# Performance work log

Hardware: AMD Instinct MI355X
Metric: run time of the kernel (lower is better)

Reference implementation:

```python
import jax, jax.numpy as jnp
import numpy as np

EMBED_DIM = 64  # scale factor dim (matches head dim)


def setup_inputs() -> dict:
    key0 = jax.random.key(0)
    kq, kk, kv = jax.random.split(key0, 3)
    shape = (2, 16, 2048, 64)  # [B, H, S, D]
    return {
        "query": jax.random.normal(kq, shape, dtype=jnp.float32),
        "key": jax.random.normal(kk, shape, dtype=jnp.float32),
        "value": jax.random.normal(kv, shape, dtype=jnp.float32),
    }


def reference(query, key, value):
    # qk = Q K^T / sqrt(embed_dim); softmax over last dim; @ V
    inv_scale = jnp.sqrt(jnp.asarray(EMBED_DIM, dtype=query.dtype))
    scores = jnp.einsum("bhqd,bhkd->bhqk", query, key) / inv_scale
    probs = jax.nn.softmax(scores, axis=-1)
    # dropout_p=0.0 -> identity (eval semantics)
    return jnp.einsum("bhqk,bhkd->bhqd", probs, value)
```

## Files before the change

### kernel.cpp

```cpp
#include <hip/hip_runtime.h>
#include <hip/hip_bf16.h>

#define S_LEN 2048
#define DDIM  64
#define NT    (S_LEN / 64)
#define SCALE  0.125f
#define SCALE2 0.18033688f
#define NELEM  4194304
#define NQROW  65536

typedef __attribute__((ext_vector_type(8))) short short8;
typedef __attribute__((ext_vector_type(4))) short short4v;
typedef __attribute__((ext_vector_type(4))) float floatx4;

__device__ __forceinline__ short f2bf(float f) {
    union { float f; unsigned u; } v; v.f = f;
    return (short)((v.u + 0x7fffu + ((v.u >> 16) & 1u)) >> 16);
}

__device__ __forceinline__ float fexp2(float x) {
#if __has_builtin(__builtin_amdgcn_exp2f)
    return __builtin_amdgcn_exp2f(x);
#else
    return exp2f(x);
#endif
}

__device__ __forceinline__ void dma16(const void* g, void* l) {
    __builtin_amdgcn_global_load_lds(
        (const __attribute__((address_space(1))) void*)g,
        (__attribute__((address_space(3))) void*)l, 16, 0, 0);
}

__global__ __launch_bounds__(256) void prep_kv(const float* __restrict__ K,
                                               const float* __restrict__ V,
                                               short* __restrict__ Kb,
                                               short* __restrict__ Vt) {
    __shared__ short T[64 * 68];
    const int bh = blockIdx.x & 31;
    const int st = blockIdx.x >> 5;
    const int t  = threadIdx.x;
    const size_t tile_off = (size_t)bh * (S_LEN * DDIM) + (size_t)st * (64 * DDIM);

    {
        const float* src = K + tile_off + t * 16;
        short* dst = Kb + tile_off + t * 16;
        #pragma unroll
        for (int h = 0; h < 2; ++h) {
            float4 a = *(const float4*)(src + h * 8);
            float4 b = *(const float4*)(src + h * 8 + 4);
            short8 o;
            o[0]=f2bf(a.x); o[1]=f2bf(a.y); o[2]=f2bf(a.z); o[3]=f2bf(a.w);
            o[4]=f2bf(b.x); o[5]=f2bf(b.y); o[6]=f2bf(b.z); o[7]=f2bf(b.w);
            *(short8*)(dst + h * 8) = o;
        }
    }

    const float* src = V + tile_off;
    const int skey = t >> 2, scol = (t & 3) * 4;
    #pragma unroll
    for (int i = 0; i < 4; ++i) {
        const int c = scol + i * 16;
        float4 v = *(const float4*)(src + (size_t)skey * 64 + c);
        short4v o; o[0]=f2bf(v.x); o[1]=f2bf(v.y); o[2]=f2bf(v.z); o[3]=f2bf(v.w);
        *(short4v*)&T[skey * 68 + c] = o;
    }
    __syncthreads();
    const int d = t >> 2, cb = (t & 3) * 16;
    short8 o0, o1;
    #pragma unroll
    for (int j = 0; j < 8; ++j) {
        o0[j] = T[(cb + j) * 68 + d];
        o1[j] = T[(cb + 8 + j) * 68 + d];
    }
    short* dst = Vt + (size_t)bh * (DDIM * S_LEN) + (size_t)d * S_LEN + st * 64 + cb;
    *(short8*)dst       = o0;
    *(short8*)(dst + 8) = o1;
}

template <int NSPLIT>
__global__ __launch_bounds__(256) void attn_sm(
    const float* __restrict__ Q, const short* __restrict__ Kb,
    const short* __restrict__ Vt, float* __restrict__ O,
    float* __restrict__ numer, float* __restrict__ denom)
{
    __shared__ short Ks[2][64 * 64];
    __shared__ short Vs[2][64 * 64];
    __shared__ short Pl[4][32 * 64];

    constexpr int NIT = NT / NSPLIT;

    const int tid  = threadIdx.x;
    const int wave = tid >> 6;
    const int lane = tid & 63;
    const int l16  = lane & 15;
    const int quad = lane >> 4;
    const int x7   = l16 & 7;

    const int bh = blockIdx.x & 31;
    const int rest = blockIdx.x >> 5;
    const int qt = rest & 15;
    const int ks = rest >> 4;
    const size_t base = (size_t)bh * (S_LEN * DDIM);

    const int ci0 = tid,        r0 = ci0 >> 3, c0 = (ci0 & 7) ^ (r0 & 7);
    const int ci1 = 256 + tid,  r1 = ci1 >> 3, c1 = (ci1 & 7) ^ (r1 & 7);
    const size_t koff = (size_t)ks * NIT * (64 * 64);
    const size_t voff = (size_t)ks * NIT * 64;
    const short* pK0 = Kb + base + koff + r0 * 64 + c0 * 8;
    const short* pK1 = Kb + base + koff + r1 * 64 + c1 * 8;
    const short* pV0 = Vt + base + voff + (size_t)r0 * S_LEN + c0 * 8;
    const short* pV1 = Vt + base + voff + (size_t)r1 * S_LEN + c1 * 8;

    dma16(pK0, &Ks[0][ci0 * 8]);
    dma16(pK1, &Ks[0][ci1 * 8]);
    dma16(pV0, &Vs[0][ci0 * 8]);
    dma16(pV1, &Vs[0][ci1 * 8]);

    short8 qf[2][2];
    #pragma unroll
    for (int nq = 0; nq < 2; ++nq) {
        const float* qp = Q + base + (size_t)(qt * 128 + wave * 32 + nq * 16 + l16) * 64 + quad * 8;
        #pragma unroll
        for (int kt = 0; kt < 2; ++kt) {
            float4 a = *(const float4*)(qp + kt * 32);
            float4 b = *(const float4*)(qp + kt * 32 + 4);
            short* d = (short*)&qf[nq][kt];
            d[0]=f2bf(a.x*SCALE2); d[1]=f2bf(a.y*SCALE2); d[2]=f2bf(a.z*SCALE2); d[3]=f2bf(a.w*SCALE2);
            d[4]=f2bf(b.x*SCALE2); d[5]=f2bf(b.y*SCALE2); d[6]=f2bf(b.z*SCALE2); d[7]=f2bf(b.w*SCALE2);
        }
    }

    floatx4 oacc[2][4];
    float rs[2];
    #pragma unroll
    for (int mt = 0; mt < 2; ++mt) {
        #pragma unroll
        for (int dt = 0; dt < 4; ++dt) oacc[mt][dt] = (floatx4){0.f,0.f,0.f,0.f};
        rs[mt] = 0.f;
    }

    short* Pw = &Pl[wave][0];

    for (int kb = 0; kb < NIT; ++kb) {
        const int cur = kb & 1;
        __syncthreads();

        if (kb + 1 < NIT) {
            const int nxt = cur ^ 1;
            const int ok = (kb + 1) * (64 * 64), ov = (kb + 1) * 64;
            dma16(pK0 + ok, &Ks[nxt][ci0 * 8]);
            dma16(pK1 + ok, &Ks[nxt][ci1 * 8]);
            dma16(pV0 + ov, &Vs[nxt][ci0 * 8]);
            dma16(pV1 + ov, &Vs[nxt][ci1 * 8]);
        }

        const short* ks_ = Ks[cur];
        floatx4 sc[2][4];
        #pragma unroll
        for (int mk = 0; mk < 4; ++mk) {
            floatx4 a0 = (floatx4){0.f,0.f,0.f,0.f};
            floatx4 a1 = (floatx4){0.f,0.f,0.f,0.f};
            #pragma unroll
            for (int kt = 0; kt < 2; ++kt) {
                const int csw = (kt * 4 + quad) ^ x7;
                short8 kf = *(const short8*)&ks_[(mk * 16 + l16) * 64 + csw * 8];
                a0 = __builtin_amdgcn_mfma_f32_16x16x32_bf16(kf, qf[0][kt], a0, 0, 0, 0);
                a1 = __builtin_amdgcn_mfma_f32_16x16x32_bf16(kf, qf[1][kt], a1, 0, 0, 0);
            }
            sc[0][mk] = a0; sc[1][mk] = a1;
        }

        #pragma unroll
        for (int nq = 0; nq < 2; ++nq) {
            const int prow = (nq * 16 + l16) * 64;
            #pragma unroll
            for (int mk = 0; mk < 4; ++mk) {
                float p0 = fexp2(sc[nq][mk][0]);
                float p1 = fexp2(sc[nq][mk][1]);
                float p2 = fexp2(sc[nq][mk][2]);
                float p3 = fexp2(sc[nq][mk][3]);
                rs[nq] += (p0 + p1) + (p2 + p3);
                short4v pv;
                pv[0]=f2bf(p0); pv[1]=f2bf(p1); pv[2]=f2bf(p2); pv[3]=f2bf(p3);
                const int c8 = (mk * 4 + quad) ^ (2 * x7);
                *(short4v*)&Pw[prow + c8 * 4] = pv;
            }
        }

        const short* vs = Vs[cur];
        #pragma unroll
        for (int kt = 0; kt < 2; ++kt) {
            const int csw = (kt * 4 + quad) ^ x7;
            short8 pf0 = *(const short8*)&Pw[(l16)      * 64 + csw * 8];
            short8 pf1 = *(const short8*)&Pw[(16 + l16) * 64 + csw * 8];
            #pragma unroll
            for (int dt = 0; dt < 4; ++dt) {
                short8 vf = *(const short8*)&vs[(dt * 16 + l16) * 64 + csw * 8];
                oacc[0][dt] = __builtin_amdgcn_mfma_f32_16x16x32_bf16(pf0, vf, oacc[0][dt], 0, 0, 0);
                oacc[1][dt] = __builtin_amdgcn_mfma_f32_16x16x32_bf16(pf1, vf, oacc[1][dt], 0, 0, 0);
            }
        }
    }

    float inv[2];
    #pragma unroll
    for (int nq = 0; nq < 2; ++nq) {
        float s = rs[nq];
        s += __shfl_xor(s, 16, 64);
        s += __shfl_xor(s, 32, 64);
        if (NSPLIT == 2) {
            if (quad == 0)
                denom[(size_t)ks * NQROW + bh * S_LEN + qt * 128 + wave * 32 + nq * 16 + l16] = s;
        }
        inv[nq] = 1.0f / s;
    }

    #pragma unroll
    for (int mt = 0; mt < 2; ++mt) {
        const float dv = (NSPLIT == 1) ? __shfl(inv[mt], quad * 4, 64) : 0.f;
        #pragma unroll
        for (int r = 0; r < 4; ++r) {
            const int row = qt * 128 + wave * 32 + mt * 16 + quad * 4 + r;
            if (NSPLIT == 1) {
                const float d_r = __shfl(inv[mt], quad * 4 + r, 64);
                float* op = O + base + (size_t)row * 64 + l16;
                #pragma unroll
                for (int dt = 0; dt < 4; ++dt)
                    op[dt * 16] = oacc[mt][dt][r] * d_r;
            } else {
                float* np = numer + (size_t)ks * NELEM + base + (size_t)row * 64 + l16;
                #pragma unroll
                for (int dt = 0; dt < 4; ++dt)
                    np[dt * 16] = oacc[mt][dt][r];
            }
        }
        (void)dv;
    }
}

__global__ __launch_bounds__(256) void combine2(const float* __restrict__ numer,
                                                const float* __restrict__ denom,
                                                float* __restrict__ O) {
    const size_t i = ((size_t)blockIdx.x * 256 + threadIdx.x) * 4;
    const size_t q = i >> 6;
    const float inv = 1.0f / (denom[q] + denom[NQROW + q]);
    float4 n0 = *(const float4*)(numer + i);
    float4 n1 = *(const float4*)(numer + NELEM + i);
    float4 o;
    o.x = (n0.x + n1.x) * inv;
    o.y = (n0.y + n1.y) * inv;
    o.z = (n0.z + n1.z) * inv;
    o.w = (n0.w + n1.w) * inv;
    *(float4*)(O + i) = o;
}

#define BQ    64
#define BKEY  64
#define KPAD  72

__global__ __launch_bounds__(256) void attn_kernel(
    const float* __restrict__ Q, const float* __restrict__ K,
    const float* __restrict__ V, float* __restrict__ O)
{
    __shared__ short Ksh[BKEY * KPAD];
    __shared__ short Vtt[DDIM * KPAD];
    __shared__ short Pls[4][16 * KPAD];

    const int tid  = threadIdx.x;
    const int wave = tid >> 6;
    const int lane = tid & 63;
    const int l16  = lane & 15;
    const int quad = lane >> 4;

    const int bh = blockIdx.x & 31;
    const int qt = blockIdx.x >> 5;
    const size_t base = (size_t)bh * S_LEN * DDIM;

    const int qrow = qt * BQ + wave * 16 + l16;
    short8 qf[2];
    {
        const float* qp = Q + base + (size_t)qrow * DDIM + quad * 8;
        #pragma unroll
        for (int kt = 0; kt < 2; ++kt) {
            float4 a = *(const float4*)(qp + kt * 32);
            float4 b = *(const float4*)(qp + kt * 32 + 4);
            short* d = (short*)&qf[kt];
            d[0]=f2bf(a.x*SCALE); d[1]=f2bf(a.y*SCALE); d[2]=f2bf(a.z*SCALE); d[3]=f2bf(a.w*SCALE);
            d[4]=f2bf(b.x*SCALE); d[5]=f2bf(b.y*SCALE); d[6]=f2bf(b.z*SCALE); d[7]=f2bf(b.w*SCALE);
        }
    }

    float m_i[4], l_i[4];
    floatx4 oacc[4];
    #pragma unroll
    for (int r = 0; r < 4; ++r) { m_i[r] = -3.0e38f; l_i[r] = 0.f; }
    #pragma unroll
    for (int dt = 0; dt < 4; ++dt) oacc[dt] = (floatx4){0.f, 0.f, 0.f, 0.f};

    const int skey = tid >> 2;
    const int scol = (tid & 3) * 4;

    for (int kb = 0; kb < S_LEN / BKEY; ++kb) {
        const float* Kg = K + base + (size_t)kb * BKEY * DDIM + (size_t)skey * DDIM;
        const float* Vg = V + base + (size_t)kb * BKEY * DDIM + (size_t)skey * DDIM;
        #pragma unroll
        for (int i = 0; i < 4; ++i) {
            const int c = scol + i * 16;
            float4 kv = *(const float4*)(Kg + c);
            short* kd = &Ksh[skey * KPAD + c];
            kd[0]=f2bf(kv.x); kd[1]=f2bf(kv.y); kd[2]=f2bf(kv.z); kd[3]=f2bf(kv.w);
            float4 vv = *(const float4*)(Vg + c);
            Vtt[(c+0)*KPAD + skey] = f2bf(vv.x);
            Vtt[(c+1)*KPAD + skey] = f2bf(vv.y);
            Vtt[(c+2)*KPAD + skey] = f2bf(vv.z);
            Vtt[(c+3)*KPAD + skey] = f2bf(vv.w);
        }
        __syncthreads();

        floatx4 sc[4];
        #pragma unroll
        for (int nt = 0; nt < 4; ++nt) {
            floatx4 acc = (floatx4){0.f, 0.f, 0.f, 0.f};
            #pragma unroll
            for (int kt = 0; kt < 2; ++kt) {
                short8 kf = *(const short8*)&Ksh[(nt*16 + l16) * KPAD + kt*32 + quad*8];
                acc = __builtin_amdgcn_mfma_f32_16x16x32_bf16(qf[kt], kf, acc, 0, 0, 0);
            }
            sc[nt] = acc;
        }

        short* Pw = &Pls[wave][0];
        #pragma unroll
        for (int r = 0; r < 4; ++r) {
            float mx = fmaxf(fmaxf(sc[0][r], sc[1][r]), fmaxf(sc[2][r], sc[3][r]));
            #pragma unroll
            for (int off = 1; off < 16; off <<= 1)
                mx = fmaxf(mx, __shfl_xor(mx, off, 64));
            const float mnew  = fmaxf(m_i[r], mx);
            const float alpha = __expf(m_i[r] - mnew);
            m_i[r] = mnew;
            float rsum = 0.f;
            #pragma unroll
            for (int nt = 0; nt < 4; ++nt) {
                float p = __expf(sc[nt][r] - mnew);
                rsum += p;
                Pw[(quad*4 + r) * KPAD + nt*16 + l16] = f2bf(p);
            }
            #pragma unroll
            for (int off = 1; off < 16; off <<= 1)
                rsum += __shfl_xor(rsum, off, 64);
            l_i[r] = l_i[r] * alpha + rsum;
            oacc[0][r] *= alpha; oacc[1][r] *= alpha;
            oacc[2][r] *= alpha; oacc[3][r] *= alpha;
        }

        #pragma unroll
        for (int kt = 0; kt < 2; ++kt) {
            short8 pf = *(const short8*)&Pw[l16 * KPAD + kt*32 + quad*8];
            #pragma unroll
            for (int dt = 0; dt < 4; ++dt) {
                short8 vf = *(const short8*)&Vtt[(dt*16 + l16) * KPAD + kt*32 + quad*8];
                oacc[dt] = __builtin_amdgcn_mfma_f32_16x16x32_bf16(pf, vf, oacc[dt], 0, 0, 0);
            }
        }
        __syncthreads();
    }

    #pragma unroll
    for (int r = 0; r < 4; ++r) {
        const float inv = 1.0f / l_i[r];
        const int row = qt * BQ + wave * 16 + quad * 4 + r;
        float* op = O + base + (size_t)row * DDIM + l16;
        #pragma unroll
        for (int dt = 0; dt < 4; ++dt)
            op[dt * 16] = oacc[dt][r] * inv;
    }
}

extern "C" void kernel_launch(void* const* d_in, const int* in_sizes, int n_in,
                              void* d_out, int out_size, void* d_ws, size_t ws_size,
                              hipStream_t stream) {
    const float* Q = (const float*)d_in[0];
    const float* K = (const float*)d_in[1];
    const float* V = (const float*)d_in[2];
    float* O = (float*)d_out;

    const size_t prep_bytes = (size_t)NELEM * 2 * 2;
    const size_t split_bytes = prep_bytes + (size_t)2 * NELEM * 4
                             + (size_t)2 * NQROW * 4;

    if (ws_size >= split_bytes) {
        short* Kb  = (short*)d_ws;
        short* Vtp = (short*)d_ws + NELEM;
        float* num = (float*)((char*)d_ws + prep_bytes);
        float* den = num + (size_t)2 * NELEM;
        prep_kv<<<dim3(1024), dim3(256), 0, stream>>>(K, V, Kb, Vtp);
        attn_sm<2><<<dim3(1024), dim3(256), 0, stream>>>(Q, Kb, Vtp, nullptr, num, den);
        combine2<<<dim3(NELEM / 1024), dim3(256), 0, stream>>>(num, den, O);
    } else if (ws_size >= prep_bytes) {
        short* Kb  = (short*)d_ws;
        short* Vtp = (short*)d_ws + NELEM;
        prep_kv<<<dim3(1024), dim3(256), 0, stream>>>(K, V, Kb, Vtp);
        attn_sm<1><<<dim3(512), dim3(256), 0, stream>>>(Q, Kb, Vtp, O, nullptr, nullptr);
    } else {
        attn_kernel<<<dim3(1024), dim3(256), 0, stream>>>(Q, K, V, O);
    }
}
```

Baseline: 158.0 us.

## Single-buffer V tile loaded mid-iteration and use packed bf16 conversion

The V tile in LDS goes from double to single buffering. It is now loaded at the start of each iteration, overlapped with the QK^T and softmax phase, and a second __syncthreads is added before the PV MFMAs. This cuts LDS use from 40KB to 32KB per block, which could allow more resident blocks, at the cost of an extra barrier and less latency hiding for V. Scalar float-to-bf16 rounding is also replaced with a packed two-value conversion intrinsic where one is available, to reduce ALU work in the prep, Q-load and P-store paths.

```diff
diff --git a/kernel.cpp b/kernel.cpp
--- a/kernel.cpp
+++ b/kernel.cpp
@@ -16,6 +16,18 @@
 __device__ __forceinline__ short f2bf(float f) {
     union { float f; unsigned u; } v; v.f = f;
     return (short)((v.u + 0x7fffu + ((v.u >> 16) & 1u)) >> 16);
+}
+
+__device__ __forceinline__ unsigned pk2bf(float a, float b) {
+#if __has_builtin(__builtin_amdgcn_cvt_pk_bf16_f32)
+    auto r = __builtin_amdgcn_cvt_pk_bf16_f32(a, b);
+    union { decltype(r) v; unsigned u; } c; c.v = r; return c.u;
+#else
+    union { float f; unsigned u; } x, y; x.f = a; y.f = b;
+    unsigned lo = (x.u + 0x7fffu + ((x.u >> 16) & 1u)) >> 16;
+    unsigned hi = (y.u + 0x7fffu + ((y.u >> 16) & 1u)) & 0xffff0000u;
+    return lo | hi;
+#endif
 }
 
 __device__ __forceinline__ float fexp2(float x) {
@@ -49,10 +61,10 @@
         for (int h = 0; h < 2; ++h) {
             float4 a = *(const float4*)(src + h * 8);
             float4 b = *(const float4*)(src + h * 8 + 4);
-            short8 o;
-            o[0]=f2bf(a.x); o[1]=f2bf(a.y); o[2]=f2bf(a.z); o[3]=f2bf(a.w);
-            o[4]=f2bf(b.x); o[5]=f2bf(b.y); o[6]=f2bf(b.z); o[7]=f2bf(b.w);
-            *(short8*)(dst + h * 8) = o;
+            uint4 o;
+            o.x = pk2bf(a.x, a.y); o.y = pk2bf(a.z, a.w);
+            o.z = pk2bf(b.x, b.y); o.w = pk2bf(b.z, b.w);
+            *(uint4*)(dst + h * 8) = o;
         }
     }
 
@@ -62,8 +74,8 @@
     for (int i = 0; i < 4; ++i) {
         const int c = scol + i * 16;
         float4 v = *(const float4*)(src + (size_t)skey * 64 + c);
-        short4v o; o[0]=f2bf(v.x); o[1]=f2bf(v.y); o[2]=f2bf(v.z); o[3]=f2bf(v.w);
-        *(short4v*)&T[skey * 68 + c] = o;
+        uint2 o; o.x = pk2bf(v.x, v.y); o.y = pk2bf(v.z, v.w);
+        *(uint2*)&T[skey * 68 + c] = o;
     }
     __syncthreads();
     const int d = t >> 2, cb = (t & 3) * 16;
@@ -85,7 +97,7 @@
     float* __restrict__ numer, float* __restrict__ denom)
 {
     __shared__ short Ks[2][64 * 64];
-    __shared__ short Vs[2][64 * 64];
+    __shared__ short Vs[64 * 64];
     __shared__ short Pl[4][32 * 64];
 
     constexpr int NIT = NT / NSPLIT;
@@ -114,8 +126,6 @@
 
     dma16(pK0, &Ks[0][ci0 * 8]);
     dma16(pK1, &Ks[0][ci1 * 8]);
-    dma16(pV0, &Vs[0][ci0 * 8]);
-    dma16(pV1, &Vs[0][ci1 * 8]);
 
     short8 qf[2][2];
     #pragma unroll
@@ -125,9 +135,12 @@
         for (int kt = 0; kt < 2; ++kt) {
             float4 a = *(const float4*)(qp + kt * 32);
             float4 b = *(const float4*)(qp + kt * 32 + 4);
-            short* d = (short*)&qf[nq][kt];
-            d[0]=f2bf(a.x*SCALE2); d[1]=f2bf(a.y*SCALE2); d[2]=f2bf(a.z*SCALE2); d[3]=f2bf(a.w*SCALE2);
-            d[4]=f2bf(b.x*SCALE2); d[5]=f2bf(b.y*SCALE2); d[6]=f2bf(b.z*SCALE2); d[7]=f2bf(b.w*SCALE2);
+            union { unsigned u[4]; short8 s; } qc;
+            qc.u[0] = pk2bf(a.x * SCALE2, a.y * SCALE2);
+            qc.u[1] = pk2bf(a.z * SCALE2, a.w * SCALE2);
+            qc.u[2] = pk2bf(b.x * SCALE2, b.y * SCALE2);
+            qc.u[3] = pk2bf(b.z * SCALE2, b.w * SCALE2);
+            qf[nq][kt] = qc.s;
         }
     }
 
@@ -146,13 +159,15 @@
         const int cur = kb & 1;
         __syncthreads();
 
+        {
+            const int ov = kb * 64;
+            dma16(pV0 + ov, &Vs[ci0 * 8]);
+            dma16(pV1 + ov, &Vs[ci1 * 8]);
+        }
         if (kb + 1 < NIT) {
-            const int nxt = cur ^ 1;
-            const int ok = (kb + 1) * (64 * 64), ov = (kb + 1) * 64;
-            dma16(pK0 + ok, &Ks[nxt][ci0 * 8]);
-            dma16(pK1 + ok, &Ks[nxt][ci1 * 8]);
-            dma16(pV0 + ov, &Vs[nxt][ci0 * 8]);
-            dma16(pV1 + ov, &Vs[nxt][ci1 * 8]);
+            const int ok = (kb + 1) * (64 * 64);
+            dma16(pK0 + ok, &Ks[cur ^ 1][ci0 * 8]);
+            dma16(pK1 + ok, &Ks[cur ^ 1][ci1 * 8]);
         }
 
         const short* ks_ = Ks[cur];
@@ -181,14 +196,14 @@
                 float p2 = fexp2(sc[nq][mk][2]);
                 float p3 = fexp2(sc[nq][mk][3]);
                 rs[nq] += (p0 + p1) + (p2 + p3);
-                short4v pv;
-                pv[0]=f2bf(p0); pv[1]=f2bf(p1); pv[2]=f2bf(p2); pv[3]=f2bf(p3);
+                uint2 pv; pv.x = pk2bf(p0, p1); pv.y = pk2bf(p2, p3);
                 const int c8 = (mk * 4 + quad) ^ (2 * x7);
-                *(short4v*)&Pw[prow + c8 * 4] = pv;
-            }
-        }
-
-        const short* vs = Vs[cur];
+                *(uint2*)&Pw[prow + c8 * 4] = pv;
+            }
+        }
+
+        __syncthreads();
+
         #pragma unroll
         for (int kt = 0; kt < 2; ++kt) {
             const int csw = (kt * 4 + quad) ^ x7;
@@ -196,7 +211,7 @@
             short8 pf1 = *(const short8*)&Pw[(16 + l16) * 64 + csw * 8];
             #pragma unroll
             for (int dt = 0; dt < 4; ++dt) {
-                short8 vf = *(const short8*)&vs[(dt * 16 + l16) * 64 + csw * 8];
+                short8 vf = *(const short8*)&Vs[(dt * 16 + l16) * 64 + csw * 8];
                 oacc[0][dt] = __builtin_amdgcn_mfma_f32_16x16x32_bf16(pf0, vf, oacc[0][dt], 0, 0, 0);
                 oacc[1][dt] = __builtin_amdgcn_mfma_f32_16x16x32_bf16(pf1, vf, oacc[1][dt], 0, 0, 0);
             }
@@ -218,7 +233,6 @@
 
     #pragma unroll
     for (int mt = 0; mt < 2; ++mt) {
-        const float dv = (NSPLIT == 1) ? __shfl(inv[mt], quad * 4, 64) : 0.f;
         #pragma unroll
         for (int r = 0; r < 4; ++r) {
             const int row = qt * 128 + wave * 32 + mt * 16 + quad * 4 + r;
@@ -235,7 +249,6 @@
                     np[dt * 16] = oacc[mt][dt][r];
             }
         }
-        (void)dv;
     }
 }
 
```

Result: no change. 160.9 us (+1.8%).
